# Performance work log

Measured on AMD Instinct MI355X. Metric: run time of the kernel, lower is better.

## Reference

```python
import jax, jax.numpy as jnp
import numpy as np
from jax import lax

STRIDES = (8, 16, 32, 64, 128)
LEVEL_HW = ((100, 128), (50, 64), (25, 32), (13, 16), (7, 8))
NUM_CLASSES = 80
PRE_NMS_THRESH = 0.05
PRE_NMS_TOPK = 1000
NMS_THRESH = 0.6
MAX_DET = 100
CLS_OFFSET = 1.0e4  # > max image coordinate, separates classes for joint NMS


def setup_inputs() -> dict:
    key = jax.random.key(0)
    B = 16
    ks = jax.random.split(key, 3 * len(LEVEL_HW))
    inp = {}
    i = 0
    for lvl, (h, w) in enumerate(LEVEL_HW):
        # shift logits down so sigmoid scores are mostly below the 0.05 candidate
        # threshold (realistic detection sparsity)
        inp[f"logits_p{lvl + 3}"] = jax.random.normal(ks[i], (B, NUM_CLASSES, h, w), jnp.float32) - 4.0; i += 1
        inp[f"bbox_p{lvl + 3}"] = jax.random.uniform(ks[i], (B, 4, h, w), jnp.float32, minval=0.0, maxval=64.0); i += 1
        inp[f"ctr_p{lvl + 3}"] = jax.random.normal(ks[i], (B, 1, h, w), jnp.float32); i += 1
    inp["im_info"] = jnp.tile(jnp.array([[800.0, 1024.0]], jnp.float32), (B, 1))
    return inp


def _locations(h, w, stride):
    # FCOSLocation: center of each stride cell -> [HW, 2] as (x, y)
    sx = jnp.arange(w, dtype=jnp.float32) * stride + stride // 2
    sy = jnp.arange(h, dtype=jnp.float32) * stride + stride // 2
    yy, xx = jnp.meshgrid(sy, sx, indexing="ij")
    return jnp.stack([xx.reshape(-1), yy.reshape(-1)], axis=-1)


def _nms_single(boxes, scores, classes):
    # boxes [K,4], scores [K] (descending), classes [K] int
    off = classes.astype(jnp.float32)[:, None] * CLS_OFFSET
    nb = boxes + off  # class-offset trick -> per-class NMS in one pass
    areas = jnp.maximum(nb[:, 2] - nb[:, 0], 0.0) * jnp.maximum(nb[:, 3] - nb[:, 1], 0.0)

    def body(sc, _):
        i = jnp.argmax(sc)
        s = sc[i]
        bi = nb[i]
        xx1 = jnp.maximum(bi[0], nb[:, 0])
        yy1 = jnp.maximum(bi[1], nb[:, 1])
        xx2 = jnp.minimum(bi[2], nb[:, 2])
        yy2 = jnp.minimum(bi[3], nb[:, 3])
        inter = jnp.maximum(xx2 - xx1, 0.0) * jnp.maximum(yy2 - yy1, 0.0)
        iou = inter / (areas[i] + areas - inter + 1e-9)
        sc2 = jnp.where(iou >= NMS_THRESH, -jnp.inf, sc).at[i].set(-jnp.inf)
        return sc2, (i, s > 0.0)

    _, (idxs, valid) = lax.scan(body, scores, None, length=MAX_DET)
    det = jnp.concatenate(
        [boxes[idxs], scores[idxs][:, None], classes[idxs].astype(jnp.float32)[:, None]],
        axis=-1,
    )  # [MAX_DET, 6] = x1,y1,x2,y2,score,class
    return jnp.where(valid[:, None], det, 0.0)


def _forward(logits_p3, bbox_p3, ctr_p3, logits_p4, bbox_p4, ctr_p4,
             logits_p5, bbox_p5, ctr_p5, logits_p6, bbox_p6, ctr_p6,
             logits_p7, bbox_p7, ctr_p7, im_info):
    levels = [(logits_p3, bbox_p3, ctr_p3), (logits_p4, bbox_p4, ctr_p4),
              (logits_p5, bbox_p5, ctr_p5), (logits_p6, bbox_p6, ctr_p6),
              (logits_p7, bbox_p7, ctr_p7)]
    scores_l, boxes_l = [], []
    for (lg, rg, ct), stride in zip(levels, STRIDES):
        B, C, H, W = lg.shape
        cls = jax.nn.sigmoid(lg).transpose(0, 2, 3, 1).reshape(B, H * W, C)
        cen = jax.nn.sigmoid(ct).transpose(0, 2, 3, 1).reshape(B, H * W, 1)
        # candidate threshold on raw class prob, then modulate by centerness
        comb = jnp.where(cls > PRE_NMS_THRESH, cls * cen, 0.0)
        locs = _locations(H, W, stride)  # [HW, 2]
        reg = rg.transpose(0, 2, 3, 1).reshape(B, H * W, 4)  # (l, t, r, b)
        bx = jnp.stack([locs[None, :, 0] - reg[..., 0],
                        locs[None, :, 1] - reg[..., 1],
                        locs[None, :, 0] + reg[..., 2],
                        locs[None, :, 1] + reg[..., 3]], axis=-1)
        scores_l.append(comb)
        boxes_l.append(bx)
    scores = jnp.concatenate(scores_l, axis=1)  # [B, N, C]
    boxes = jnp.concatenate(boxes_l, axis=1)    # [B, N, 4]
    B, N, C = scores.shape
    vals, idx = lax.top_k(scores.reshape(B, N * C), PRE_NMS_TOPK)  # [B, K]
    loc = idx // C
    cls_id = idx % C
    cand = jnp.take_along_axis(boxes, loc[..., None], axis=1)  # [B, K, 4]
    h = im_info[:, 0:1]
    w = im_info[:, 1:2]
    x1 = jnp.clip(cand[..., 0], 0.0, w - 1.0)
    y1 = jnp.clip(cand[..., 1], 0.0, h - 1.0)
    x2 = jnp.clip(cand[..., 2], 0.0, w - 1.0)
    y2 = jnp.clip(cand[..., 3], 0.0, h - 1.0)
    cand = jnp.stack([x1, y1, x2, y2], axis=-1)
    sc = jnp.where(vals > 0.0, jnp.sqrt(jnp.maximum(vals, 0.0) + 1e-12), 0.0)
    return jax.vmap(_nms_single)(cand, sc, cls_id)  # [B, MAX_DET, 6]


def reference(logits_p3, bbox_p3, ctr_p3, logits_p4, bbox_p4, ctr_p4,
              logits_p5, bbox_p5, ctr_p5, logits_p6, bbox_p6, ctr_p6,
              logits_p7, bbox_p7, ctr_p7, im_info):
    return _forward(logits_p3, bbox_p3, ctr_p3, logits_p4, bbox_p4, ctr_p4,
                    logits_p5, bbox_p5, ctr_p5, logits_p6, bbox_p6, ctr_p6,
                    logits_p7, bbox_p7, ctr_p7, im_info)
```

## Files before the change

### kernel.cpp

```cpp
#include <hip/hip_runtime.h>
#include <math.h>

#pragma clang fp contract(off)

#define NB 16
#define NC 80
#define NTOT 17064
#define TOPK 1000
#define NBINS 8192
#define CAP 4096
#define MAXDET 100
#define NREP 2
#define CNTSTRIDE 64
#define CHUNK 128

struct Ptrs {
    const float* lg[5];
    const float* bb[5];
    const float* ct[5];
};

__device__ __forceinline__ void level_of(int n, int& l, int& hw, int& W,
                                         int& stride, int& half, int& HW) {
    if (n < 12800)      { l = 0; hw = n;         W = 128; stride = 8;   half = 4;  HW = 12800; }
    else if (n < 16000) { l = 1; hw = n - 12800; W = 64;  stride = 16;  half = 8;  HW = 3200;  }
    else if (n < 16800) { l = 2; hw = n - 16000; W = 32;  stride = 32;  half = 16; HW = 800;   }
    else if (n < 17008) { l = 3; hw = n - 16800; W = 16;  stride = 64;  half = 32; HW = 208;   }
    else                { l = 4; hw = n - 17008; W = 8;   stride = 128; half = 64; HW = 56;    }
}

template<int HW4, int NF4>
__device__ __forceinline__ void hist_level(const float* lgb, const float* ctb,
                                           int tid, int bx, int gx, unsigned* lh) {
    for (int i0 = bx * 256; i0 < NF4; i0 += gx * 256) {
        int i = i0 + tid;
        if (i < NF4) {
            int c   = i / HW4;
            int hwf = i - c * HW4;
            float4 v  = *(const float4*)(lgb + c * (HW4 * 4) + hwf * 4);
            if (v.x > -2.95f || v.y > -2.95f || v.z > -2.95f || v.w > -2.95f) {
                float4 cv = *(const float4*)(ctb + hwf * 4);
                float xs[4] = {v.x, v.y, v.z, v.w};
                float cs[4] = {cv.x, cv.y, cv.z, cv.w};
#pragma unroll
                for (int j = 0; j < 4; ++j) {
                    float x = xs[j];
                    if (x > -2.95f) {
                        float cls = 1.0f / (1.0f + expf(-x));
                        if (cls > 0.05f) {
                            float cen = 1.0f / (1.0f + expf(-cs[j]));
                            float comb = cls * cen;
                            atomicAdd(&lh[__float_as_uint(comb) >> 19], 1u);
                        }
                    }
                }
            }
        }
    }
}

__global__ void __launch_bounds__(256) k_histA(Ptrs p, unsigned* hist) {
    __shared__ unsigned lh[NBINS];
    int b = blockIdx.y, tid = threadIdx.x, bx = blockIdx.x, gx = gridDim.x;
    for (int i = tid; i < NBINS; i += 256) lh[i] = 0;
    __syncthreads();

    hist_level<3200, 256000>(p.lg[0] + (size_t)b * NC * 12800, p.ct[0] + (size_t)b * 12800, tid, bx, gx, lh);
    hist_level< 800,  64000>(p.lg[1] + (size_t)b * NC * 3200,  p.ct[1] + (size_t)b * 3200,  tid, bx, gx, lh);
    hist_level< 200,  16000>(p.lg[2] + (size_t)b * NC * 800,   p.ct[2] + (size_t)b * 800,   tid, bx, gx, lh);
    hist_level<  52,   4160>(p.lg[3] + (size_t)b * NC * 208,   p.ct[3] + (size_t)b * 208,   tid, bx, gx, lh);
    hist_level<  14,   1120>(p.lg[4] + (size_t)b * NC * 56,    p.ct[4] + (size_t)b * 56,    tid, bx, gx, lh);

    __syncthreads();
    unsigned* h = hist + ((size_t)(bx & (NREP - 1)) * NB + b) * NBINS;
    for (int i = tid; i < NBINS; i += 256) {
        unsigned v = lh[i];
        if (v) atomicAdd(&h[i], v);
    }
}

__global__ void __launch_bounds__(256) k_thresh(const unsigned* hist, unsigned* T) {
    __shared__ unsigned hl[NBINS];
    __shared__ unsigned wtot[4];
    __shared__ int Tf;
    int b = blockIdx.x, tid = threadIdx.x, lane = tid & 63, wv = tid >> 6;
    if (tid == 0) Tf = 0;
    for (int i = tid; i < NBINS; i += 256) {
        unsigned s = 0;
        for (int r = 0; r < NREP; ++r)
            s += hist[((size_t)r * NB + b) * NBINS + i];
        hl[i] = s;
    }
    __syncthreads();
    int base = tid * 32;
    unsigned mysum = 0;
#pragma unroll
    for (int i = 0; i < 32; ++i) mysum += hl[base + i];
    unsigned incl = mysum;
#pragma unroll
    for (int off = 1; off < 64; off <<= 1) {
        unsigned v = __shfl_down(incl, off);
        if (lane + off < 64) incl += v;
    }
    if (lane == 0) wtot[wv] = incl;
    __syncthreads();
    unsigned above = 0;
    for (int w = wv + 1; w < 4; ++w) above += wtot[w];
    unsigned sufincl = incl + above;
    unsigned excl = sufincl - mysum;
    if (excl < TOPK && sufincl >= TOPK) {
        unsigned running = excl;
        for (int bin = base + 31; bin >= base; --bin) {
            running += hl[bin];
            if (running >= TOPK) { Tf = bin; break; }
        }
    }
    __syncthreads();
    if (tid == 0) T[b] = (unsigned)Tf;
}

template<int HW4, int NF4, int LVOFF>
__device__ __forceinline__ void compact_level(const float* lgb, const float* ctb,
        int tid, int lane, int bx, int gx, unsigned Tb, float xpre,
        unsigned* cntb, unsigned long long* selb, unsigned long long ltmask) {
    for (int i0 = bx * 256; i0 < NF4; i0 += gx * 256) {
        int i = i0 + tid;
        bool f0 = false, f1 = false, f2 = false, f3 = false;
        unsigned long long k0 = 0, k1 = 0, k2 = 0, k3 = 0;
        if (i < NF4) {
            int c   = i / HW4;
            int hwf = i - c * HW4;
            float4 v = *(const float4*)(lgb + c * (HW4 * 4) + hwf * 4);
            if (v.x > xpre || v.y > xpre || v.z > xpre || v.w > xpre) {
                float4 cv = *(const float4*)(ctb + hwf * 4);
                int nbase = LVOFF + hwf * 4;
#define DO_J(J, X, CT, F, K)                                                  \
                if ((X) > xpre) {                                             \
                    float cls = 1.0f / (1.0f + expf(-(X)));                   \
                    if (cls > 0.05f) {                                        \
                        float cen = 1.0f / (1.0f + expf(-(CT)));              \
                        float comb = cls * cen;                               \
                        unsigned bits = __float_as_uint(comb);                \
                        if ((bits >> 19) >= Tb) {                             \
                            unsigned idx = (unsigned)((nbase + (J)) * NC + c);\
                            K = ((unsigned long long)bits << 32) |            \
                                (0xFFFFFFFFu - idx);                          \
                            F = true;                                         \
                        }                                                     \
                    }                                                         \
                }
                DO_J(0, v.x, cv.x, f0, k0)
                DO_J(1, v.y, cv.y, f1, k1)
                DO_J(2, v.z, cv.z, f2, k2)
                DO_J(3, v.w, cv.w, f3, k3)
#undef DO_J
            }
        }
        unsigned long long m0 = __ballot(f0), m1 = __ballot(f1);
        unsigned long long m2 = __ballot(f2), m3 = __ballot(f3);
        if ((m0 | m1 | m2 | m3) == 0ULL) continue;
        unsigned t0 = (unsigned)__popcll(m0), t1 = (unsigned)__popcll(m1);
        unsigned t2 = (unsigned)__popcll(m2), t3 = (unsigned)__popcll(m3);
        unsigned total = t0 + t1 + t2 + t3;
        int basep = 0;
        if (lane == 0) basep = (int)atomicAdd(cntb, total);
        basep = __shfl(basep, 0);
        if (f0) { int pos = basep + (int)__popcll(m0 & ltmask);                       if (pos < CAP) selb[pos] = k0; }
        if (f1) { int pos = basep + (int)t0 + (int)__popcll(m1 & ltmask);             if (pos < CAP) selb[pos] = k1; }
        if (f2) { int pos = basep + (int)(t0 + t1) + (int)__popcll(m2 & ltmask);      if (pos < CAP) selb[pos] = k2; }
        if (f3) { int pos = basep + (int)(t0 + t1 + t2) + (int)__popcll(m3 & ltmask); if (pos < CAP) selb[pos] = k3; }
    }
}

__global__ void __launch_bounds__(256) k_compactB(Ptrs p, const unsigned* T,
                                                  unsigned* cnt2, unsigned long long* sel) {
    int b = blockIdx.y, tid = threadIdx.x, lane = tid & 63;
    int bx = blockIdx.x, gx = gridDim.x;
    unsigned Tb = T[b];
    float mthr = __uint_as_float(Tb << 19);
    float xpre = -2.95f;
    if (mthr > 1e-37f && mthr < 1.0f) {
        float lm = logf(mthr / (1.0f - mthr)) - 0.01f;
        if (lm > xpre) xpre = lm;
    }
    unsigned long long ltmask = (1ULL << lane) - 1ULL;
    unsigned* cntb = cnt2 + (size_t)b * CNTSTRIDE;
    unsigned long long* selb = sel + (size_t)b * CAP;
    compact_level<3200, 256000,     0>(p.lg[0] + (size_t)b * NC * 12800, p.ct[0] + (size_t)b * 12800, tid, lane, bx, gx, Tb, xpre, cntb, selb, ltmask);
    compact_level< 800,  64000, 12800>(p.lg[1] + (size_t)b * NC * 3200,  p.ct[1] + (size_t)b * 3200,  tid, lane, bx, gx, Tb, xpre, cntb, selb, ltmask);
    compact_level< 200,  16000, 16000>(p.lg[2] + (size_t)b * NC * 800,   p.ct[2] + (size_t)b * 800,   tid, lane, bx, gx, Tb, xpre, cntb, selb, ltmask);
    compact_level<  52,   4160, 16800>(p.lg[3] + (size_t)b * NC * 208,   p.ct[3] + (size_t)b * 208,   tid, lane, bx, gx, Tb, xpre, cntb, selb, ltmask);
    compact_level<  14,   1120, 17008>(p.lg[4] + (size_t)b * NC * 56,    p.ct[4] + (size_t)b * 56,    tid, lane, bx, gx, Tb, xpre, cntb, selb, ltmask);
}

__global__ void __launch_bounds__(256) k_rankdec(Ptrs p, const unsigned* cnt,
                                                 const unsigned long long* sel,
                                                 const float* im_info, float* cand) {
    __shared__ __align__(16) unsigned long long keys[CAP];
    int b = blockIdx.y, tid = threadIdx.x;
    unsigned M = cnt[(size_t)b * CNTSTRIDE];
    if (M > CAP) M = CAP;
    int s0 = blockIdx.x * 256;
    if (s0 >= (int)M) return;
    int Mpad = (int)((M + 1u) & ~1u);
    for (int i = tid; i < Mpad; i += 256)
        keys[i] = (i < (int)M) ? sel[(size_t)b * CAP + i] : 0ULL;
    __syncthreads();

    int s = s0 + tid;
    if (s >= (int)M) return;
    unsigned long long k = keys[s];
    int rank = 0;
    for (int j = 0; j < Mpad; j += 2) {
        ulonglong2 kk = *(const ulonglong2*)&keys[j];
        rank += (kk.x > k) ? 1 : 0;
        rank += (kk.y > k) ? 1 : 0;
    }
    if (rank >= TOPK) return;

    float Him = im_info[b * 2 + 0], Wim = im_info[b * 2 + 1];
    float xmax = Wim - 1.0f, ymax = Him - 1.0f;
    unsigned sb = (unsigned)(k >> 32);
    unsigned idx = 0xFFFFFFFFu - (unsigned)(k & 0xFFFFFFFFu);
    float val = __uint_as_float(sb);
    int n = idx / NC, c = idx - n * NC;
    int l, hw, W, stride, half, HW;
    level_of(n, l, hw, W, stride, half, HW);
    int wx = hw % W, hy = hw / W;
    float locx = (float)(wx * stride + half);
    float locy = (float)(hy * stride + half);
    const float* bb = p.bb[l] + (size_t)b * 4 * HW + hw;
    float r0 = bb[0], r1 = bb[(size_t)HW], r2 = bb[(size_t)2 * HW], r3 = bb[(size_t)3 * HW];
    float x1 = locx - r0, y1 = locy - r1, x2 = locx + r2, y2 = locy + r3;
    x1 = fminf(fmaxf(x1, 0.f), xmax);
    y1 = fminf(fmaxf(y1, 0.f), ymax);
    x2 = fminf(fmaxf(x2, 0.f), xmax);
    y2 = fminf(fmaxf(y2, 0.f), ymax);
    float scv = sqrtf(val + 1e-12f);
    float off = (float)c * 10000.0f;
    float a0 = x1 + off, a1 = y1 + off, a2 = x2 + off, a3 = y2 + off;
    float area = fmaxf(a2 - a0, 0.f) * fmaxf(a3 - a1, 0.f);
    float* dst = cand + ((size_t)b * TOPK + rank) * 12;
    *(float4*)(dst + 0) = make_float4(x1, y1, x2, y2);
    *(float4*)(dst + 4) = make_float4(a0, a1, a2, a3);
    *(float4*)(dst + 8) = make_float4(area, scv, (float)c, 0.f);
}

__global__ void __launch_bounds__(64) k_nms(const unsigned* cnt, const float* cand,
                                            float* out) {
    __shared__ float4 s_ob[CHUNK], s_nb[CHUNK], s_ms[CHUNK];
    int b = blockIdx.x, lane = threadIdx.x;
    unsigned M = cnt[(size_t)b * CNTSTRIDE];
    if (M > CAP) M = CAP;
    int ncand = (int)M < TOPK ? (int)M : TOPK;
    const float* src = cand + (size_t)b * TOPK * 12;
    float* ob = out + (size_t)b * MAXDET * 6;

    int na = 0;
    float4 a0b = make_float4(0.f, 0.f, 0.f, 0.f);
    float4 a1b = make_float4(0.f, 0.f, 0.f, 0.f);
    float a0a = 0.f, a1a = 0.f;

    for (int base = 0; base < ncand && na < MAXDET; base += CHUNK) {
        int cn = ncand - base; if (cn > CHUNK) cn = CHUNK;
        for (int cidx = lane; cidx < cn; cidx += 64) {
            const float* s = src + (size_t)(base + cidx) * 12;
            s_ob[cidx] = *(const float4*)(s + 0);
            s_nb[cidx] = *(const float4*)(s + 4);
            s_ms[cidx] = *(const float4*)(s + 8);
        }
        __syncthreads();
        for (int r = 0; r < cn && na < MAXDET; ++r) {
            float4 cb = s_nb[r];
            float ca = s_ms[r].x;
            bool sup = false;
            if (lane < na) {
                float xx1 = fmaxf(a0b.x, cb.x);
                float yy1 = fmaxf(a0b.y, cb.y);
                float xx2 = fminf(a0b.z, cb.z);
                float yy2 = fminf(a0b.w, cb.w);
                float inter = fmaxf(xx2 - xx1, 0.f) * fmaxf(yy2 - yy1, 0.f);
                float iou = inter / (((a0a + ca) - inter) + 1e-9f);
                sup = (iou >= 0.6f);
            }
            if (lane + 64 < na) {
                float xx1 = fmaxf(a1b.x, cb.x);
                float yy1 = fmaxf(a1b.y, cb.y);
                float xx2 = fminf(a1b.z, cb.z);
                float yy2 = fminf(a1b.w, cb.w);
                float inter = fmaxf(xx2 - xx1, 0.f) * fmaxf(yy2 - yy1, 0.f);
                float iou = inter / (((a1a + ca) - inter) + 1e-9f);
                sup |= (iou >= 0.6f);
            }
            if (__ballot(sup) == 0ULL) {
                if (lane == (na & 63)) {
                    if (na < 64) { a0b = cb; a0a = ca; }
                    else         { a1b = cb; a1a = ca; }
                }
                if (lane == 0) {
                    float4 o4 = s_ob[r]; float4 m4 = s_ms[r];
                    ob[na * 6 + 0] = o4.x; ob[na * 6 + 1] = o4.y;
                    ob[na * 6 + 2] = o4.z; ob[na * 6 + 3] = o4.w;
                    ob[na * 6 + 4] = m4.y; ob[na * 6 + 5] = m4.z;
                }
                ++na;
            }
        }
        __syncthreads();
    }
    for (int q = na * 6 + lane; q < MAXDET * 6; q += 64)
        ob[q] = 0.f;
}

extern "C" void kernel_launch(void* const* d_in, const int* in_sizes, int n_in,
                              void* d_out, int out_size, void* d_ws, size_t ws_size,
                              hipStream_t stream) {
    Ptrs p;
    for (int l = 0; l < 5; ++l) {
        p.lg[l] = (const float*)d_in[3 * l + 0];
        p.bb[l] = (const float*)d_in[3 * l + 1];
        p.ct[l] = (const float*)d_in[3 * l + 2];
    }
    const float* im_info = (const float*)d_in[15];
    float* out = (float*)d_out;

    unsigned char* w = (unsigned char*)d_ws;
    unsigned* hist          = (unsigned*)(w);
    unsigned* cnt2          = (unsigned*)(w + 1048576);
    unsigned* T             = (unsigned*)(w + 1052672);
    unsigned long long* sel = (unsigned long long*)(w + 1052928);
    float* cand             = (float*)(w + 1577216);

    hipMemsetAsync(w, 0, 1052928, stream);

    k_histA<<<dim3(64, NB), 256, 0, stream>>>(p, hist);
    k_thresh<<<NB, 256, 0, stream>>>(hist, T);
    k_compactB<<<dim3(128, NB), 256, 0, stream>>>(p, T, cnt2, sel);
    k_rankdec<<<dim3(16, NB), 256, 0, stream>>>(p, cnt2, sel, im_info, cand);
    k_nms<<<NB, 64, 0, stream>>>(cnt2, cand, out);
}
```

Before: 255.0 us.

## Fuse candidate compaction into histogram pass and filter from per-wave segments

The histogram kernel now also writes every candidate above the pre-NMS threshold into per-wave segment buffers, keyed by score bits and index. A new filter kernel then reads only these segments against the threshold instead of rescanning all logits in a second compaction pass. This is meant to remove a second full read of the large logit tensors. It also adds fast sigmoid with an exact-recheck band, 16-bit packed shared histogram bins, and more global histogram replicas. It requires a large workspace and falls back to the old path if the workspace is too small. Segments that overflow are truncated, which could drop candidates.

Result: no change. 257.2 us (+0.9%).

```diff
diff --git a/kernel.cpp b/kernel.cpp
--- a/kernel.cpp
+++ b/kernel.cpp
@@ -10,9 +10,12 @@
 #define NBINS 8192
 #define CAP 4096
 #define MAXDET 100
-#define NREP 2
+#define NREP 4
 #define CNTSTRIDE 64
 #define CHUNK 128
+#define G1 128
+#define NSEG 512
+#define SEGW 1024
 
 struct Ptrs {
     const float* lg[5];
@@ -29,52 +32,100 @@
     else                { l = 4; hw = n - 17008; W = 8;   stride = 128; half = 64; HW = 56;    }
 }
 
-template<int HW4, int NF4>
-__device__ __forceinline__ void hist_level(const float* lgb, const float* ctb,
-                                           int tid, int bx, int gx, unsigned* lh) {
+__device__ __forceinline__ float fast_sig(float x) {
+    float e = __expf(-x);
+    return __builtin_amdgcn_rcpf(1.0f + e);
+}
+
+template<int HW4, int NF4, int LVOFF, bool WRITE>
+__device__ __forceinline__ void sweep_level(const float* lgb, const float* ctb,
+        int tid, int lane, int bx, int gx, unsigned* lh32,
+        unsigned long long* segp, unsigned& cur, unsigned long long ltmask) {
     for (int i0 = bx * 256; i0 < NF4; i0 += gx * 256) {
         int i = i0 + tid;
+        bool f0 = false, f1 = false, f2 = false, f3 = false;
+        unsigned long long k0 = 0, k1 = 0, k2 = 0, k3 = 0;
         if (i < NF4) {
             int c   = i / HW4;
             int hwf = i - c * HW4;
             float4 v  = *(const float4*)(lgb + c * (HW4 * 4) + hwf * 4);
             if (v.x > -2.95f || v.y > -2.95f || v.z > -2.95f || v.w > -2.95f) {
                 float4 cv = *(const float4*)(ctb + hwf * 4);
-                float xs[4] = {v.x, v.y, v.z, v.w};
-                float cs[4] = {cv.x, cv.y, cv.z, cv.w};
-#pragma unroll
-                for (int j = 0; j < 4; ++j) {
-                    float x = xs[j];
-                    if (x > -2.95f) {
-                        float cls = 1.0f / (1.0f + expf(-x));
-                        if (cls > 0.05f) {
-                            float cen = 1.0f / (1.0f + expf(-cs[j]));
-                            float comb = cls * cen;
-                            atomicAdd(&lh[__float_as_uint(comb) >> 19], 1u);
-                        }
-                    }
-                }
-            }
-        }
-    }
-}
-
-__global__ void __launch_bounds__(256) k_histA(Ptrs p, unsigned* hist) {
-    __shared__ unsigned lh[NBINS];
+                int nbase = LVOFF + hwf * 4;
+#define DO_J(J, X, CT, F, K)                                                  \
+                if ((X) > -2.95f) {                \
+                    float cls = fast_sig(X);                                  \
+                    if (cls > 0.04999f) {                                     \
+                        bool in = true;                                       \
+                        if (cls < 0.05001f)      \
+                            in = (1.0f / (1.0f + expf(-(X)))) > 0.05f;        \
+                        if (in) {                                             \
+                            float cen = fast_sig(CT);                         \
+                            float comb = cls * cen;                           \
+                            unsigned bits = __float_as_uint(comb);            \
+                            unsigned cb = (bits > 32u) ? bits - 32u : 0u;     \
+                            unsigned bin = cb >> 19;                          \
+                            atomicAdd(&lh32[bin >> 1],                        \
+                                      (bin & 1u) ? 0x10000u : 1u);            \
+                            if (WRITE) {                                      \
+                                unsigned idx = (unsigned)((nbase + (J)) * NC + c);\
+                                K = ((unsigned long long)bits << 32) |        \
+                                    (0xFFFFFFFFu - idx);                      \
+                                F = true;                                     \
+                            }                                                 \
+                        }                                                     \
+                    }                                                         \
+                }
+                DO_J(0, v.x, cv.x, f0, k0)
+                DO_J(1, v.y, cv.y, f1, k1)
+                DO_J(2, v.z, cv.z, f2, k2)
+                DO_J(3, v.w, cv.w, f3, k3)
+#undef DO_J
+            }
+        }
+        if (WRITE) {
+            unsigned long long m0 = __ballot(f0), m1 = __ballot(f1);
+            unsigned long long m2 = __ballot(f2), m3 = __ballot(f3);
+            if ((m0 | m1 | m2 | m3) == 0ULL) continue;
+            unsigned t0 = (unsigned)__popcll(m0), t1 = (unsigned)__popcll(m1);
+            unsigned t2 = (unsigned)__popcll(m2), t3 = (unsigned)__popcll(m3);
+            if (f0) { unsigned pos = cur + (unsigned)__popcll(m0 & ltmask);                if (pos < SEGW) segp[pos] = k0; }
+            if (f1) { unsigned pos = cur + t0 + (unsigned)__popcll(m1 & ltmask);           if (pos < SEGW) segp[pos] = k1; }
+            if (f2) { unsigned pos = cur + t0 + t1 + (unsigned)__popcll(m2 & ltmask);      if (pos < SEGW) segp[pos] = k2; }
+            if (f3) { unsigned pos = cur + t0 + t1 + t2 + (unsigned)__popcll(m3 & ltmask); if (pos < SEGW) segp[pos] = k3; }
+            cur += t0 + t1 + t2 + t3;
+        }
+    }
+}
+
+template<bool WRITE>
+__global__ void __launch_bounds__(256) k_score1(Ptrs p, unsigned* hist,
+                                                unsigned* segcnt,
+                                                unsigned long long* segbuf) {
+    __shared__ unsigned lh32[NBINS / 2];
     int b = blockIdx.y, tid = threadIdx.x, bx = blockIdx.x, gx = gridDim.x;
-    for (int i = tid; i < NBINS; i += 256) lh[i] = 0;
-    __syncthreads();
-
-    hist_level<3200, 256000>(p.lg[0] + (size_t)b * NC * 12800, p.ct[0] + (size_t)b * 12800, tid, bx, gx, lh);
-    hist_level< 800,  64000>(p.lg[1] + (size_t)b * NC * 3200,  p.ct[1] + (size_t)b * 3200,  tid, bx, gx, lh);
-    hist_level< 200,  16000>(p.lg[2] + (size_t)b * NC * 800,   p.ct[2] + (size_t)b * 800,   tid, bx, gx, lh);
-    hist_level<  52,   4160>(p.lg[3] + (size_t)b * NC * 208,   p.ct[3] + (size_t)b * 208,   tid, bx, gx, lh);
-    hist_level<  14,   1120>(p.lg[4] + (size_t)b * NC * 56,    p.ct[4] + (size_t)b * 56,    tid, bx, gx, lh);
+    int lane = tid & 63, wv = tid >> 6;
+    unsigned long long ltmask = (1ULL << lane) - 1ULL;
+    for (int i = tid; i < NBINS / 2; i += 256) lh32[i] = 0;
+    __syncthreads();
+
+    unsigned long long* segp = WRITE
+        ? segbuf + (((size_t)b * G1 + bx) * 4 + wv) * SEGW : nullptr;
+    unsigned cur = 0;
+
+    sweep_level<3200, 256000,     0, WRITE>(p.lg[0] + (size_t)b * NC * 12800, p.ct[0] + (size_t)b * 12800, tid, lane, bx, gx, lh32, segp, cur, ltmask);
+    sweep_level< 800,  64000, 12800, WRITE>(p.lg[1] + (size_t)b * NC * 3200,  p.ct[1] + (size_t)b * 3200,  tid, lane, bx, gx, lh32, segp, cur, ltmask);
+    sweep_level< 200,  16000, 16000, WRITE>(p.lg[2] + (size_t)b * NC * 800,   p.ct[2] + (size_t)b * 800,   tid, lane, bx, gx, lh32, segp, cur, ltmask);
+    sweep_level<  52,   4160, 16800, WRITE>(p.lg[3] + (size_t)b * NC * 208,   p.ct[3] + (size_t)b * 208,   tid, lane, bx, gx, lh32, segp, cur, ltmask);
+    sweep_level<  14,   1120, 17008, WRITE>(p.lg[4] + (size_t)b * NC * 56,    p.ct[4] + (size_t)b * 56,    tid, lane, bx, gx, lh32, segp, cur, ltmask);
+
+    if (WRITE && lane == 0)
+        segcnt[(size_t)b * NSEG + bx * 4 + wv] = (cur < SEGW) ? cur : SEGW;
 
     __syncthreads();
     unsigned* h = hist + ((size_t)(bx & (NREP - 1)) * NB + b) * NBINS;
     for (int i = tid; i < NBINS; i += 256) {
-        unsigned v = lh[i];
+        unsigned v = (lh32[i >> 1] >> ((i & 1) * 16)) & 0xFFFFu;
         if (v) atomicAdd(&h[i], v);
     }
 }
@@ -117,6 +168,55 @@
     }
     __syncthreads();
     if (tid == 0) T[b] = (unsigned)Tf;
+}
+
+__global__ void __launch_bounds__(256) k_filter(Ptrs p, const unsigned* T,
+                                                const unsigned* segcnt,
+                                                const unsigned long long* segbuf,
+                                                unsigned* cnt2, unsigned long long* sel) {
+    int b = blockIdx.y, tid = threadIdx.x, lane = tid & 63;
+    unsigned Tb = T[b];
+    unsigned Tshift = Tb << 19;
+    unsigned fmin = (Tshift >= 32u) ? Tshift - 32u : 0u;
+    unsigned long long ltmask = (1ULL << lane) - 1ULL;
+    unsigned* cntb = cnt2 + (size_t)b * CNTSTRIDE;
+    unsigned long long* selb = sel + (size_t)b * CAP;
+
+    for (int sg = blockIdx.x * 16; sg < blockIdx.x * 16 + 16; ++sg) {
+        unsigned sc = segcnt[(size_t)b * NSEG + sg];
+        const unsigned long long* src = segbuf + ((size_t)b * NSEG + sg) * SEGW;
+        for (int i = tid; i < (int)sc; i += 256) {
+            unsigned long long e = src[i];
+            bool f = false;
+            unsigned long long key = 0;
+            if ((unsigned)(e >> 32) >= fmin) {
+                unsigned idx = 0xFFFFFFFFu - (unsigned)(e & 0xFFFFFFFFu);
+                int n = idx / NC, c = idx - n * NC;
+                int l, hw, W, stride, half, HW;
+                level_of(n, l, hw, W, stride, half, HW);
+                float x  = p.lg[l][(size_t)b * NC * HW + (size_t)c * HW + hw];
+                float ct = p.ct[l][(size_t)b * HW + hw];
+                float cls = 1.0f / (1.0f + expf(-x));
+                float cen = 1.0f / (1.0f + expf(-ct));
+                unsigned be = __float_as_uint(cls * cen);
+                if ((be >> 19) >= Tb) {
+                    key = ((unsigned long long)be << 32) | (e & 0xFFFFFFFFULL);
+                    f = true;
+                }
+            }
+            unsigned long long mk = __ballot(f);
+            if (mk) {
+                unsigned nw = (unsigned)__popcll(mk);
+                int basep = 0;
+                if (lane == 0) basep = (int)atomicAdd(cntb, nw);
+                basep = __shfl(basep, 0);
+                if (f) {
+                    int pos = basep + (int)__popcll(mk & ltmask);
+                    if (pos < CAP) selb[pos] = key;
+                }
+            }
+        }
+    }
 }
 
 template<int HW4, int NF4, int LVOFF>
@@ -326,16 +426,25 @@
 
     unsigned char* w = (unsigned char*)d_ws;
     unsigned* hist          = (unsigned*)(w);
-    unsigned* cnt2          = (unsigned*)(w + 1048576);
-    unsigned* T             = (unsigned*)(w + 1052672);
-    unsigned long long* sel = (unsigned long long*)(w + 1052928);
-    float* cand             = (float*)(w + 1577216);
-
-    hipMemsetAsync(w, 0, 1052928, stream);
-
-    k_histA<<<dim3(64, NB), 256, 0, stream>>>(p, hist);
-    k_thresh<<<NB, 256, 0, stream>>>(hist, T);
-    k_compactB<<<dim3(128, NB), 256, 0, stream>>>(p, T, cnt2, sel);
+    unsigned* cnt2          = (unsigned*)(w + 2097152);
+    unsigned* T             = (unsigned*)(w + 2101248);
+    unsigned long long* sel = (unsigned long long*)(w + 2101504);
+    float* cand             = (float*)(w + 2625792);
+    unsigned* segcnt        = (unsigned*)(w + 3393792);
+    unsigned long long* segbuf = (unsigned long long*)(w + 3426560);
+    const bool big = ws_size >= (size_t)70535424;
+
+    hipMemsetAsync(w, 0, 2101504, stream);
+
+    if (big) {
+        k_score1<true ><<<dim3(G1, NB), 256, 0, stream>>>(p, hist, segcnt, segbuf);
+        k_thresh<<<NB, 256, 0, stream>>>(hist, T);
+        k_filter<<<dim3(NSEG / 16, NB), 256, 0, stream>>>(p, T, segcnt, segbuf, cnt2, sel);
+    } else {
+        k_score1<false><<<dim3(G1, NB), 256, 0, stream>>>(p, hist, nullptr, nullptr);
+        k_thresh<<<NB, 256, 0, stream>>>(hist, T);
+        k_compactB<<<dim3(128, NB), 256, 0, stream>>>(p, T, cnt2, sel);
+    }
     k_rankdec<<<dim3(16, NB), 256, 0, stream>>>(p, cnt2, sel, im_info, cand);
     k_nms<<<NB, 64, 0, stream>>>(cnt2, cand, out);
 }
```
